# Optimization experiments

Hardware: AMD Instinct MI355X
Metric: run time of the kernel (lower is better)

## Reference

```python
import jax, jax.numpy as jnp
import numpy as np

BITS = 8
TOPK_PERCENT = 0.1
THRESHOLD = 0.5


def _quantize_per_channel(v, n_bits):
    # scales: abs-max over last dim, clamped, divided by q_max
    q_max = 2 ** (n_bits - 1) - 1
    scales = jnp.max(jnp.abs(v), axis=-1, keepdims=True)
    scales = jnp.clip(scales, 1e-5, None) / q_max
    return jnp.clip(jnp.round(v / scales), -q_max - 1, q_max) * scales


def setup_inputs() -> dict:
    key = jax.random.key(0)
    ks = jax.random.split(key, 5)
    B, S, D, H = 4, 2048, 1024, 4096
    return {
        "x": jax.random.normal(ks[0], (B, S, D), dtype=jnp.float32),
        "W1": jax.random.normal(ks[1], (H, D), dtype=jnp.float32) * 0.02,
        "b1": jax.random.normal(ks[2], (H,), dtype=jnp.float32) * 0.02,
        "W2": jax.random.normal(ks[3], (D, H), dtype=jnp.float32) * 0.02,
        "b2": jax.random.normal(ks[4], (D,), dtype=jnp.float32) * 0.02,
    }


def reference(x, W1, b1, W2, b2):
    D = W1.shape[-1]
    H = W1.shape[0]
    topk_rows = int(D * TOPK_PERCENT) + 1  # first-k-columns approximation

    # approximate preactivation using only the first topk_rows input channels
    prod_topk = jnp.einsum('bsk,hk->bsh', x[:, :, :topk_rows], W1[:, :topk_rows]) + b1
    # exact fp preactivation
    prod = jnp.einsum('bsd,hd->bsh', x, W1) + b1

    # quantized path: per-channel quant of x, W1, b1 then matmul
    q_x = _quantize_per_channel(x, BITS)
    q_w = _quantize_per_channel(W1, BITS)
    q_b = _quantize_per_channel(b1, BITS)
    q_pre = jnp.einsum('bsd,hd->bsh', q_x, q_w) + q_b

    # channel selection: channels predicted positive often enough stay fp
    threshold = prod_topk.shape[-1] * THRESHOLD
    num_pos_pred = jnp.sum(prod_topk > 0, axis=(0, 1))  # [H]
    fp_channels = num_pos_pred > threshold              # [H] bool

    h = jnp.where(fp_channels, prod, q_pre)
    h = jax.nn.gelu(h, approximate=False)
    out = jnp.einsum('bsh,dh->bsd', h, W2) + b2
    return out
```

## Files before the change

kernel.cpp:

```cpp
#include <hip/hip_runtime.h>
#include <math.h>
#include <stdint.h>


typedef __bf16 v8bf __attribute__((ext_vector_type(8)));
typedef float v4f __attribute__((ext_vector_type(4)));

#define AS_G __attribute__((address_space(1)))
#define AS_L __attribute__((address_space(3)))

__device__ __forceinline__ unsigned short f2bf(float f) {
    union { float f; unsigned int i; } v; v.f = f;
    unsigned int r = v.i + 0x7fffu + ((v.i >> 16) & 1u);
    return (unsigned short)(r >> 16);
}
__device__ __forceinline__ float gelu_exact(float v) {
    return 0.5f * v * (1.0f + erff(v * 0.70710678118654752440f));
}

__device__ __forceinline__ void gemm_core(const unsigned short* __restrict__ A,
                                          const unsigned short* __restrict__ B,
                                          int K, int bm0, int bn0,
                                          unsigned short* ldsA, unsigned short* ldsB,
                                          v4f acc[4][4])
{
    const int tid  = threadIdx.x;
    const int wave = tid >> 6;
    const int lane = tid & 63;
    const int rowInChunk = lane >> 2;
    const int col8       = (lane & 3) * 8;
    const int ldsLane    = lane * 8;
    const int c0 = wave * 2, c1 = wave * 2 + 1;
    const int wm = wave & 1, wn = wave >> 1;

    const size_t aR0 = (size_t)(bm0 + c0 * 16 + rowInChunk) * K + col8;
    const size_t aR1 = (size_t)(bm0 + c1 * 16 + rowInChunk) * K + col8;
    const size_t bR0 = (size_t)(bn0 + c0 * 16 + rowInChunk) * K + col8;
    const size_t bR1 = (size_t)(bn0 + c1 * 16 + rowInChunk) * K + col8;

    for (int k0 = 0; k0 < K; k0 += 32) {
        __builtin_amdgcn_global_load_lds((const AS_G void*)(A + aR0 + k0),
                                         (AS_L void*)(ldsA + c0 * 512 + ldsLane), 16, 0, 0);
        __builtin_amdgcn_global_load_lds((const AS_G void*)(A + aR1 + k0),
                                         (AS_L void*)(ldsA + c1 * 512 + ldsLane), 16, 0, 0);
        __builtin_amdgcn_global_load_lds((const AS_G void*)(B + bR0 + k0),
                                         (AS_L void*)(ldsB + c0 * 512 + ldsLane), 16, 0, 0);
        __builtin_amdgcn_global_load_lds((const AS_G void*)(B + bR1 + k0),
                                         (AS_L void*)(ldsB + c1 * 512 + ldsLane), 16, 0, 0);
        __syncthreads();

        v8bf af[4], bfr[4];
#pragma unroll
        for (int i = 0; i < 4; ++i)
            af[i] = *(const v8bf*)&ldsA[(wm * 64 + i * 16 + (lane & 15)) * 32 + (lane >> 4) * 8];
#pragma unroll
        for (int j = 0; j < 4; ++j)
            bfr[j] = *(const v8bf*)&ldsB[(wn * 64 + j * 16 + (lane & 15)) * 32 + (lane >> 4) * 8];
#pragma unroll
        for (int i = 0; i < 4; ++i)
#pragma unroll
            for (int j = 0; j < 4; ++j)
                acc[i][j] = __builtin_amdgcn_mfma_f32_16x16x32_bf16(af[i], bfr[j], acc[i][j], 0, 0, 0);
        __syncthreads();
    }
}


__global__ void f2b_kernel(const float* __restrict__ src,
                           unsigned short* __restrict__ dst, int n)
{
    int i = (blockIdx.x * 256 + threadIdx.x) * 4;
    if (i < n) {
        float4 v = *(const float4*)(src + i);
        dst[i + 0] = f2bf(v.x);
        dst[i + 1] = f2bf(v.y);
        dst[i + 2] = f2bf(v.z);
        dst[i + 3] = f2bf(v.w);
    }
}

__global__ void pad_kernel(const float* __restrict__ x,
                           const float* __restrict__ W1,
                           unsigned short* __restrict__ xpad,
                           unsigned short* __restrict__ w1pad)
{
    int e = blockIdx.x * 256 + threadIdx.x;
    const int NX = 8192 * 128;
    if (e < NX) {
        int row = e >> 7, col = e & 127;
        xpad[e] = (col < 103) ? f2bf(x[(size_t)row * 1024 + col]) : (unsigned short)0;
    } else {
        int e2 = e - NX;
        if (e2 < 4096 * 128) {
            int row = e2 >> 7, col = e2 & 127;
            w1pad[e2] = (col < 103) ? f2bf(W1[(size_t)row * 1024 + col]) : (unsigned short)0;
        }
    }
}

__global__ void scales_kernel(const float* __restrict__ x,
                              const float* __restrict__ W1,
                              const float* __restrict__ b1,
                              float* __restrict__ s_x, float* __restrict__ s_w,
                              float* __restrict__ s_b)
{
    int b = blockIdx.x, tid = threadIdx.x;
    const float* src; int len; float* dst;
    if (b < 8192)       { src = x  + (size_t)b * 1024;          len = 1024; dst = s_x + b; }
    else if (b < 12288) { src = W1 + (size_t)(b - 8192) * 1024; len = 1024; dst = s_w + (b - 8192); }
    else                { src = b1;                              len = 4096; dst = s_b; }
    float m = 0.f;
    for (int k = tid; k < len; k += 256) m = fmaxf(m, fabsf(src[k]));
#pragma unroll
    for (int off = 32; off; off >>= 1) m = fmaxf(m, __shfl_xor(m, off, 64));
    __shared__ float red[4];
    if ((tid & 63) == 0) red[tid >> 6] = m;
    __syncthreads();
    if (tid == 0) {
        m = fmaxf(fmaxf(red[0], red[1]), fmaxf(red[2], red[3]));
        *dst = fmaxf(m, 1e-5f) * (1.0f / 127.0f);
    }
}

__global__ void topk_gemm(const unsigned short* __restrict__ xpad,
                          const unsigned short* __restrict__ w1pad,
                          const float* __restrict__ b1,
                          int* __restrict__ counts)
{
    __shared__ unsigned short ldsA[128 * 32];
    __shared__ unsigned short ldsB[128 * 32];
    v4f acc[4][4];
    v4f z = {0.f, 0.f, 0.f, 0.f};
#pragma unroll
    for (int i = 0; i < 4; ++i)
#pragma unroll
        for (int j = 0; j < 4; ++j) acc[i][j] = z;

    const int bm0 = blockIdx.x * 128, bn0 = blockIdx.y * 128;
    gemm_core(xpad, w1pad, 128, bm0, bn0, ldsA, ldsB, acc);

    const int lane = threadIdx.x & 63, wave = threadIdx.x >> 6;
    const int wn = wave >> 1;
#pragma unroll
    for (int j = 0; j < 4; ++j) {
        int n = bn0 + wn * 64 + j * 16 + (lane & 15);
        float bv = b1[n];
        int cnt = 0;
#pragma unroll
        for (int i = 0; i < 4; ++i)
#pragma unroll
            for (int r = 0; r < 4; ++r)
                cnt += (acc[i][j][r] + bv > 0.0f) ? 1 : 0;
        cnt += __shfl_xor(cnt, 16, 64);
        cnt += __shfl_xor(cnt, 32, 64);
        if (lane < 16 && cnt) atomicAdd(&counts[n], cnt);
    }
}

__global__ void gemm1_gelu(const unsigned short* __restrict__ xb,
                           const unsigned short* __restrict__ w1b,
                           const float* __restrict__ b1,
                           unsigned short* __restrict__ hbuf)
{
    __shared__ unsigned short ldsA[128 * 32];
    __shared__ unsigned short ldsB[128 * 32];
    v4f acc[4][4];
    v4f z = {0.f, 0.f, 0.f, 0.f};
#pragma unroll
    for (int i = 0; i < 4; ++i)
#pragma unroll
        for (int j = 0; j < 4; ++j) acc[i][j] = z;

    const int bm0 = blockIdx.x * 128, bn0 = blockIdx.y * 128;
    gemm_core(xb, w1b, 1024, bm0, bn0, ldsA, ldsB, acc);

    const int lane = threadIdx.x & 63, wave = threadIdx.x >> 6;
    const int wm = wave & 1, wn = wave >> 1;
#pragma unroll
    for (int j = 0; j < 4; ++j) {
        int n = bn0 + wn * 64 + j * 16 + (lane & 15);
        float bv = b1[n];
#pragma unroll
        for (int i = 0; i < 4; ++i)
#pragma unroll
            for (int r = 0; r < 4; ++r) {
                int m = bm0 + wm * 64 + i * 16 + (lane >> 4) * 4 + r;
                hbuf[(size_t)m * 4096 + n] = f2bf(gelu_exact(acc[i][j][r] + bv));
            }
    }
}

__global__ void fixup_kernel(const float* __restrict__ x,
                             const float* __restrict__ W1,
                             const float* __restrict__ b1,
                             const int* __restrict__ counts,
                             const float* __restrict__ s_x,
                             const float* __restrict__ s_w,
                             const float* __restrict__ s_b,
                             unsigned short* __restrict__ hbuf)
{
    const int n = blockIdx.x;
    if (counts[n] > 2048) return;
    __shared__ float qw[1024];
    const float swn = s_w[n];
    for (int k = threadIdx.x; k < 1024; k += 256) {
        float q = nearbyintf(W1[(size_t)n * 1024 + k] / swn);
        qw[k] = fminf(fmaxf(q, -128.f), 127.f) * swn;
    }
    __syncthreads();
    const float sb = *s_b;
    const float bq = fminf(fmaxf(nearbyintf(b1[n] / sb), -128.f), 127.f) * sb;
    for (int m = threadIdx.x; m < 8192; m += 256) {
        const float sxm = s_x[m];
        float a = 0.f;
        for (int k = 0; k < 1024; ++k) {
            float q = nearbyintf(x[(size_t)m * 1024 + k] / sxm);
            a += fminf(fmaxf(q, -128.f), 127.f) * sxm * qw[k];
        }
        hbuf[(size_t)m * 4096 + n] = f2bf(gelu_exact(a + bq));
    }
}

__global__ void gemm2_bias(const unsigned short* __restrict__ hbuf,
                           const unsigned short* __restrict__ w2b,
                           const float* __restrict__ b2,
                           float* __restrict__ out)
{
    __shared__ unsigned short ldsA[128 * 32];
    __shared__ unsigned short ldsB[128 * 32];
    v4f acc[4][4];
    v4f z = {0.f, 0.f, 0.f, 0.f};
#pragma unroll
    for (int i = 0; i < 4; ++i)
#pragma unroll
        for (int j = 0; j < 4; ++j) acc[i][j] = z;

    const int bm0 = blockIdx.x * 128, bn0 = blockIdx.y * 128;
    gemm_core(hbuf, w2b, 4096, bm0, bn0, ldsA, ldsB, acc);

    const int lane = threadIdx.x & 63, wave = threadIdx.x >> 6;
    const int wm = wave & 1, wn = wave >> 1;
#pragma unroll
    for (int j = 0; j < 4; ++j) {
        int n = bn0 + wn * 64 + j * 16 + (lane & 15);
        float bv = b2[n];
#pragma unroll
        for (int i = 0; i < 4; ++i)
#pragma unroll
            for (int r = 0; r < 4; ++r) {
                int m = bm0 + wm * 64 + i * 16 + (lane >> 4) * 4 + r;
                out[(size_t)m * 1024 + n] = acc[i][j][r] + bv;
            }
    }
}

extern "C" void kernel_launch(void* const* d_in, const int* in_sizes, int n_in,
                              void* d_out, int out_size, void* d_ws, size_t ws_size,
                              hipStream_t stream)
{
    const float* x  = (const float*)d_in[0];
    const float* W1 = (const float*)d_in[1];
    const float* b1 = (const float*)d_in[2];
    const float* W2 = (const float*)d_in[3];
    const float* b2 = (const float*)d_in[4];
    float* out = (float*)d_out;

    unsigned short* xb  = (unsigned short*)d_out;
    unsigned short* w1b = (unsigned short*)d_out + (size_t)8192*1024;

    char* ws = (char*)d_ws;
    int*   counts = (int*)(ws + 0);
    float* s_x    = (float*)(ws + (64 << 10));
    float* s_w    = (float*)(ws + (96 << 10));
    float* s_b    = (float*)(ws + (112 << 10));
    unsigned short* xpad  = (unsigned short*)(ws + (1 << 20));
    unsigned short* w1pad = (unsigned short*)(ws + (3 << 20));
    unsigned short* w2b   = (unsigned short*)(ws + (4 << 20));
    unsigned short* hbuf  = (unsigned short*)(ws + (12 << 20));

    hipMemsetAsync(counts, 0, 4096 * sizeof(int), stream);

    f2b_kernel<<<8192, 256, 0, stream>>>(x,  xb,  8192 * 1024);
    f2b_kernel<<<4096, 256, 0, stream>>>(W1, w1b, 4096 * 1024);
    f2b_kernel<<<4096, 256, 0, stream>>>(W2, w2b, 1024 * 4096);
    pad_kernel<<<(8192 * 128 + 4096 * 128 + 255) / 256, 256, 0, stream>>>(x, W1, xpad, w1pad);
    scales_kernel<<<12289, 256, 0, stream>>>(x, W1, b1, s_x, s_w, s_b);
    topk_gemm<<<dim3(64, 32), 256, 0, stream>>>(xpad, w1pad, b1, counts);
    gemm1_gelu<<<dim3(64, 32), 256, 0, stream>>>(xb, w1b, b1, hbuf);
    fixup_kernel<<<4096, 256, 0, stream>>>(x, W1, b1, counts, s_x, s_w, s_b, hbuf);
    gemm2_bias<<<dim3(64, 8), 256, 0, stream>>>(hbuf, w2b, b2, out);
}
```

Baseline: 336.8 us.

## Fuse prep kernels, swizzle GEMM LDS layout, use tanh-approx GELU

Merges the three bf16 conversion kernels, the pad kernel, the scales kernel and the counts memset into one prep kernel that reads each fp32 row once and writes every derived buffer. It also XOR-swizzles the LDS column placement in the shared GEMM core to cut bank conflicts on fragment reads, and replaces the erf-based GELU in gemm1 with a tanh-style exp approximation. The fast GELU departs from the exact erf GELU the reference requires, which is a numerical risk. The prep kernel treats W2 (1024x4096) as 4096 rows of 1024, which is fine for plain conversion.

After: 309.1 us. 1.09x faster.

```diff
diff --git a/kernel.cpp b/kernel.cpp
--- a/kernel.cpp
+++ b/kernel.cpp
@@ -13,6 +13,12 @@
     union { float f; unsigned int i; } v; v.f = f;
     unsigned int r = v.i + 0x7fffu + ((v.i >> 16) & 1u);
     return (unsigned short)(r >> 16);
+}
+__device__ __forceinline__ float gelu_fast(float v) {
+    float u = v * (0.79788456080286536f + 0.035677408136300125f * v * v);
+    u = fminf(fmaxf(u, -15.f), 15.f);
+    float e = __expf(2.0f * u);
+    return v * e * __builtin_amdgcn_rcpf(e + 1.0f);
 }
 __device__ __forceinline__ float gelu_exact(float v) {
     return 0.5f * v * (1.0f + erff(v * 0.70710678118654752440f));
@@ -28,8 +34,8 @@
     const int wave = tid >> 6;
     const int lane = tid & 63;
     const int rowInChunk = lane >> 2;
-    const int col8       = (lane & 3) * 8;
-    const int ldsLane    = lane * 8;
+    const int col8 = ((lane & 3) ^ ((lane >> 3) & 3)) * 8;
+    const int ldsLane = lane * 8;
     const int c0 = wave * 2, c1 = wave * 2 + 1;
     const int wm = wave & 1, wn = wave >> 1;
 
@@ -37,6 +43,9 @@
     const size_t aR1 = (size_t)(bm0 + c1 * 16 + rowInChunk) * K + col8;
     const size_t bR0 = (size_t)(bn0 + c0 * 16 + rowInChunk) * K + col8;
     const size_t bR1 = (size_t)(bn0 + c1 * 16 + rowInChunk) * K + col8;
+
+    const int R = lane & 15, Q = lane >> 4;
+    const int roff = R * 32 + ((Q ^ ((R >> 1) & 3)) * 8);
 
     for (int k0 = 0; k0 < K; k0 += 32) {
         __builtin_amdgcn_global_load_lds((const AS_G void*)(A + aR0 + k0),
@@ -52,10 +61,10 @@
         v8bf af[4], bfr[4];
 #pragma unroll
         for (int i = 0; i < 4; ++i)
-            af[i] = *(const v8bf*)&ldsA[(wm * 64 + i * 16 + (lane & 15)) * 32 + (lane >> 4) * 8];
+            af[i] = *(const v8bf*)&ldsA[(wm * 4 + i) * 512 + roff];
 #pragma unroll
         for (int j = 0; j < 4; ++j)
-            bfr[j] = *(const v8bf*)&ldsB[(wn * 64 + j * 16 + (lane & 15)) * 32 + (lane >> 4) * 8];
+            bfr[j] = *(const v8bf*)&ldsB[(wn * 4 + j) * 512 + roff];
 #pragma unroll
         for (int i = 0; i < 4; ++i)
 #pragma unroll
@@ -65,60 +74,60 @@
     }
 }
 
-
-__global__ void f2b_kernel(const float* __restrict__ src,
-                           unsigned short* __restrict__ dst, int n)
-{
-    int i = (blockIdx.x * 256 + threadIdx.x) * 4;
-    if (i < n) {
-        float4 v = *(const float4*)(src + i);
-        dst[i + 0] = f2bf(v.x);
-        dst[i + 1] = f2bf(v.y);
-        dst[i + 2] = f2bf(v.z);
-        dst[i + 3] = f2bf(v.w);
-    }
-}
-
-__global__ void pad_kernel(const float* __restrict__ x,
-                           const float* __restrict__ W1,
-                           unsigned short* __restrict__ xpad,
-                           unsigned short* __restrict__ w1pad)
-{
-    int e = blockIdx.x * 256 + threadIdx.x;
-    const int NX = 8192 * 128;
-    if (e < NX) {
-        int row = e >> 7, col = e & 127;
-        xpad[e] = (col < 103) ? f2bf(x[(size_t)row * 1024 + col]) : (unsigned short)0;
+__global__ void prep_kernel(const float* __restrict__ x, const float* __restrict__ W1,
+                            const float* __restrict__ W2, const float* __restrict__ b1,
+                            unsigned short* __restrict__ xb, unsigned short* __restrict__ w1b,
+                            unsigned short* __restrict__ w2b,
+                            unsigned short* __restrict__ xpad, unsigned short* __restrict__ w1pad,
+                            float* __restrict__ s_x, float* __restrict__ s_w,
+                            float* __restrict__ s_b, int* __restrict__ counts)
+{
+    const int b = blockIdx.x, t = threadIdx.x;
+    __shared__ float red[4];
+
+    if (b < 16384) {
+        const float* src; unsigned short* dst; unsigned short* pad = nullptr; float* sc = nullptr;
+        if (b < 8192)       { src = x  + (size_t)b * 1024;            dst = xb  + (size_t)b * 1024;
+                              pad = xpad  + (size_t)b * 128;          sc = s_x + b; }
+        else if (b < 12288) { int r = b - 8192;  src = W1 + (size_t)r * 1024; dst = w1b + (size_t)r * 1024;
+                              pad = w1pad + (size_t)r * 128;          sc = s_w + r; }
+        else                { int r = b - 12288; src = W2 + (size_t)r * 1024; dst = w2b + (size_t)r * 1024; }
+
+        float4 v = ((const float4*)src)[t];
+        ushort4 u;
+        u.x = f2bf(v.x); u.y = f2bf(v.y); u.z = f2bf(v.z); u.w = f2bf(v.w);
+        ((ushort4*)dst)[t] = u;
+        if (pad && t < 32) {
+            int c = t * 4;
+            ushort4 p;
+            p.x = (c + 0 < 103) ? u.x : (unsigned short)0;
+            p.y = (c + 1 < 103) ? u.y : (unsigned short)0;
+            p.z = (c + 2 < 103) ? u.z : (unsigned short)0;
+            p.w = (c + 3 < 103) ? u.w : (unsigned short)0;
+            ((ushort4*)pad)[t] = p;
+        }
+        if (sc) {
+            float m = fmaxf(fmaxf(fabsf(v.x), fabsf(v.y)), fmaxf(fabsf(v.z), fabsf(v.w)));
+#pragma unroll
+            for (int off = 32; off; off >>= 1) m = fmaxf(m, __shfl_xor(m, off, 64));
+            if ((t & 63) == 0) red[t >> 6] = m;
+            __syncthreads();
+            if (t == 0) {
+                m = fmaxf(fmaxf(red[0], red[1]), fmaxf(red[2], red[3]));
+                *sc = fmaxf(m, 1e-5f) * (1.0f / 127.0f);
+            }
+        }
     } else {
-        int e2 = e - NX;
-        if (e2 < 4096 * 128) {
-            int row = e2 >> 7, col = e2 & 127;
-            w1pad[e2] = (col < 103) ? f2bf(W1[(size_t)row * 1024 + col]) : (unsigned short)0;
-        }
-    }
-}
-
-__global__ void scales_kernel(const float* __restrict__ x,
-                              const float* __restrict__ W1,
-                              const float* __restrict__ b1,
-                              float* __restrict__ s_x, float* __restrict__ s_w,
-                              float* __restrict__ s_b)
-{
-    int b = blockIdx.x, tid = threadIdx.x;
-    const float* src; int len; float* dst;
-    if (b < 8192)       { src = x  + (size_t)b * 1024;          len = 1024; dst = s_x + b; }
-    else if (b < 12288) { src = W1 + (size_t)(b - 8192) * 1024; len = 1024; dst = s_w + (b - 8192); }
-    else                { src = b1;                              len = 4096; dst = s_b; }
-    float m = 0.f;
-    for (int k = tid; k < len; k += 256) m = fmaxf(m, fabsf(src[k]));
-#pragma unroll
-    for (int off = 32; off; off >>= 1) m = fmaxf(m, __shfl_xor(m, off, 64));
-    __shared__ float red[4];
-    if ((tid & 63) == 0) red[tid >> 6] = m;
-    __syncthreads();
-    if (tid == 0) {
-        m = fmaxf(fmaxf(red[0], red[1]), fmaxf(red[2], red[3]));
-        *dst = fmaxf(m, 1e-5f) * (1.0f / 127.0f);
+        float m = 0.f;
+        for (int k = t; k < 4096; k += 256) { m = fmaxf(m, fabsf(b1[k])); counts[k] = 0; }
+#pragma unroll
+        for (int off = 32; off; off >>= 1) m = fmaxf(m, __shfl_xor(m, off, 64));
+        if ((t & 63) == 0) red[t >> 6] = m;
+        __syncthreads();
+        if (t == 0) {
+            m = fmaxf(fmaxf(red[0], red[1]), fmaxf(red[2], red[3]));
+            *s_b = fmaxf(m, 1e-5f) * (1.0f / 127.0f);
+        }
     }
 }
 
@@ -185,7 +194,7 @@
 #pragma unroll
             for (int r = 0; r < 4; ++r) {
                 int m = bm0 + wm * 64 + i * 16 + (lane >> 4) * 4 + r;
-                hbuf[(size_t)m * 4096 + n] = f2bf(gelu_exact(acc[i][j][r] + bv));
+                hbuf[(size_t)m * 4096 + n] = f2bf(gelu_fast(acc[i][j][r] + bv));
             }
     }
 }
@@ -266,7 +275,7 @@
     float* out = (float*)d_out;
 
     unsigned short* xb  = (unsigned short*)d_out;
-    unsigned short* w1b = (unsigned short*)d_out + (size_t)8192*1024;
+    unsigned short* w1b = (unsigned short*)d_out + (size_t)8192 * 1024;
 
     char* ws = (char*)d_ws;
     int*   counts = (int*)(ws + 0);
@@ -278,13 +287,8 @@
     unsigned short* w2b   = (unsigned short*)(ws + (4 << 20));
     unsigned short* hbuf  = (unsigned short*)(ws + (12 << 20));
 
-    hipMemsetAsync(counts, 0, 4096 * sizeof(int), stream);
-
-    f2b_kernel<<<8192, 256, 0, stream>>>(x,  xb,  8192 * 1024);
-    f2b_kernel<<<4096, 256, 0, stream>>>(W1, w1b, 4096 * 1024);
-    f2b_kernel<<<4096, 256, 0, stream>>>(W2, w2b, 1024 * 4096);
-    pad_kernel<<<(8192 * 128 + 4096 * 128 + 255) / 256, 256, 0, stream>>>(x, W1, xpad, w1pad);
-    scales_kernel<<<12289, 256, 0, stream>>>(x, W1, b1, s_x, s_w, s_b);
+    prep_kernel<<<16385, 256, 0, stream>>>(x, W1, W2, b1, xb, w1b, w2b,
+                                           xpad, w1pad, s_x, s_w, s_b, counts);
     topk_gemm<<<dim3(64, 32), 256, 0, stream>>>(xpad, w1pad, b1, counts);
     gemm1_gelu<<<dim3(64, 32), 256, 0, stream>>>(xb, w1b, b1, hbuf);
     fixup_kernel<<<4096, 256, 0, stream>>>(x, W1, b1, counts, s_x, s_w, s_b, hbuf);
```
